# Kernel tuning notes

Hardware: AMD Instinct MI355X
Metric: run time of the kernel (lower is better)

The kernel has to match this reference:

```python
import jax, jax.numpy as jnp
import numpy as np

TEMPERATURE = 0.07
EPS = 1e-12  # F.normalize eps


def setup_inputs() -> dict:
    key = jax.random.key(0)
    kA, kB = jax.random.split(key)
    N, V, D = 4096, 2, 256
    A = jax.random.normal(kA, (N, V, D), dtype=jnp.float32)
    B = jax.random.normal(kB, (N, V, D), dtype=jnp.float32)
    return {"A": A, "B": B}


def _l2norm(x):
    n = jnp.sqrt(jnp.sum(x * x, axis=-1, keepdims=True))
    return x / jnp.maximum(n, EPS)


def _contrastive_loss(A, B, temperature):
    N, VA, D = A.shape
    VB = B.shape[1]
    # (N, V, D) -> (V*N, D), view-major, matching transpose(0,1).reshape
    Af = _l2norm(jnp.transpose(A, (1, 0, 2)).reshape(VA * N, D))
    Bf = _l2norm(jnp.transpose(B, (1, 0, 2)).reshape(VB * N, D))
    logits = Af @ Bf.T  # (VA*N, VB*N), square since VA == VB
    M = VA * N
    row = jnp.arange(M, dtype=jnp.int32)[:, None]          # (M, 1)
    cols = jnp.arange(M - 1, dtype=jnp.int32)[None, :]     # (1, M-1)
    # off-diagonal column indices for each row (skip j == i)
    cols = cols + (cols >= row).astype(jnp.int32)          # (M, M-1)
    lab = (row % N) == (cols % N)                          # positives mask
    logits_nd = jnp.take_along_axis(logits, cols, axis=1)  # diag removed
    # stable sort puts positives first (column order), negatives after ->
    # equivalent to torch.cat((pos, neg), dim=1)
    order = jnp.argsort(jnp.logical_not(lab), axis=1, stable=True)
    logits_cat = jnp.take_along_axis(logits_nd, order, axis=1) / temperature
    P = VB - 1  # positives per row after diagonal removal
    logp = jax.nn.log_softmax(logits_cat, axis=-1)
    # soft-label cross entropy: labels are 1.0 on first P columns, mean over rows
    return -jnp.mean(jnp.sum(logp[:, :P], axis=-1))


def reference(A, B):
    return _contrastive_loss(A, B, TEMPERATURE)
```

## Files before the change

kernel.cpp:

```cpp
#include <hip/hip_runtime.h>
#include <hip/hip_bf16.h>


#define N_SAMP 4096
#define DIM    256
#define M_ROWS 8192

using short8 = __attribute__((ext_vector_type(8))) short;
using f32x4  = __attribute__((ext_vector_type(4))) float;

#define GLDS(g, l) __builtin_amdgcn_global_load_lds( \
    (const __attribute__((address_space(1))) void*)(g), \
    (__attribute__((address_space(3))) void*)(l), 16, 0, 0)

__global__ __launch_bounds__(256) void norm_kernel(
    const float* __restrict__ A, const float* __restrict__ B,
    unsigned short* __restrict__ Ah, unsigned short* __restrict__ Bh,
    float* __restrict__ S)
{
  int tid = threadIdx.x;
  if (blockIdx.x < 8)
    ((float4*)S)[blockIdx.x * 256 + tid] = (float4){0.f, 0.f, 0.f, 0.f};

  int wave = tid >> 6, lane = tid & 63;
  int gw   = blockIdx.x * 4 + wave;
  const float* src; unsigned short* dst; int m;
  if (gw < M_ROWS) { src = A; dst = Ah; m = gw; }
  else             { src = B; dst = Bh; m = gw - M_ROWS; }
  int n = m & (N_SAMP - 1);
  int v = m >> 12;
  const float4* in = (const float4*)(src + (size_t)(n * 2 + v) * DIM);
  float4 x = in[lane];
  float ss = x.x*x.x + x.y*x.y + x.z*x.z + x.w*x.w;
  #pragma unroll
  for (int d = 1; d < 64; d <<= 1) ss += __shfl_xor(ss, d);
  float scale = 1.0f / fmaxf(sqrtf(ss), 1e-12f);
  float vals[4] = {x.x*scale, x.y*scale, x.z*scale, x.w*scale};
  ushort4 o;
  unsigned short* op = (unsigned short*)&o;
  #pragma unroll
  for (int k = 0; k < 4; ++k) {
    unsigned int u = __float_as_uint(vals[k]);
    u += 0x7fffu + ((u >> 16) & 1u);
    op[k] = (unsigned short)(u >> 16);
  }
  *(ushort4*)(dst + (size_t)m * DIM + lane * 4) = o;
}

__global__ __launch_bounds__(512, 2) void gemm_lse_kernel(
    const unsigned short* __restrict__ Ah, const unsigned short* __restrict__ Bh,
    float* __restrict__ S, float* __restrict__ Pos)
{
  __shared__ alignas(16) char lds[65536 + 2 * 32768];
  char* As  = lds;
  char* Bs0 = lds + 65536;
  char* Bs1 = lds + 65536 + 32768;

  int tid  = threadIdx.x;
  int lane = tid & 63;
  int w    = tid >> 6;
  int wrow = w >> 2, wcol = w & 3;
  int row0 = blockIdx.y * 128;
  int col0 = blockIdx.x * 2048;

  #pragma unroll
  for (int s = 0; s < 8; ++s) {
    int f = s * 512 + tid;
    int r = f >> 5, cd = f & 31;
    int cs = cd ^ (r & 7);
    GLDS((const char*)Ah + (size_t)(row0 + r) * 512 + cs * 16, As + f * 16);
  }
  auto stageB = [&](int t, char* Bbuf) {
    int ct = t >> 2, ks = t & 3;
    const char* base = (const char*)Bh + (size_t)(col0 + ct * 256) * 512 + ks * 128;
    #pragma unroll
    for (int s = 0; s < 4; ++s) {
      int f = s * 512 + tid;
      int r = f >> 3, cd = f & 7;
      int cs = cd ^ (r & 7);
      GLDS(base + (size_t)r * 512 + cs * 16, Bbuf + f * 16);
    }
  };
  stageB(0, Bs0);

  f32x4 acc[4][4];
  float ssum[4][4];
  #pragma unroll
  for (int i = 0; i < 4; ++i)
    #pragma unroll
    for (int r = 0; r < 4; ++r) ssum[i][r] = 0.f;

  const float KE = (float)(1.4426950408889634 / 0.07);

  for (int t = 0; t < 32; ++t) {
    char* Bcur = (t & 1) ? Bs1 : Bs0;
    char* Bnxt = (t & 1) ? Bs0 : Bs1;
    if (t < 31) {
      stageB(t + 1, Bnxt);
      asm volatile("s_waitcnt vmcnt(4)" ::: "memory");
    } else {
      asm volatile("s_waitcnt vmcnt(0)" ::: "memory");
    }
    __builtin_amdgcn_s_barrier();

    int ks = t & 3;
    if (ks == 0) {
      #pragma unroll
      for (int i = 0; i < 4; ++i)
        #pragma unroll
        for (int j = 0; j < 4; ++j)
          acc[i][j] = (f32x4){0.f, 0.f, 0.f, 0.f};
    }

    #pragma unroll
    for (int kk = 0; kk < 2; ++kk) {
      short8 a[4], b[4];
      int ca = ks * 8 + kk * 4 + (lane >> 4);
      int cb = kk * 4 + (lane >> 4);
      #pragma unroll
      for (int f = 0; f < 4; ++f) {
        int ar = wrow * 64 + f * 16 + (lane & 15);
        a[f] = *(const short8*)(As + ar * 512 + ((ca ^ (ar & 7)) * 16));
        int br = wcol * 64 + f * 16 + (lane & 15);
        b[f] = *(const short8*)(Bcur + br * 128 + ((cb ^ (br & 7)) * 16));
      }
      #pragma unroll
      for (int i = 0; i < 4; ++i)
        #pragma unroll
        for (int j = 0; j < 4; ++j)
          acc[i][j] = __builtin_amdgcn_mfma_f32_16x16x32_bf16(a[i], b[j], acc[i][j], 0, 0, 0);
    }

    if (ks == 3) {
      int ct = t >> 2;
      #pragma unroll
      for (int i = 0; i < 4; ++i) {
        #pragma unroll
        for (int j = 0; j < 4; ++j) {
          int gj = col0 + ct * 256 + wcol * 64 + j * 16 + (lane & 15);
          #pragma unroll
          for (int r = 0; r < 4; ++r) {
            int gi = row0 + wrow * 64 + i * 16 + (lane >> 4) * 4 + r;
            float l = acc[i][j][r];
            float e = exp2f(l * KE);
            if (((gi ^ gj) & (N_SAMP - 1)) == 0) {
              if (gi == gj) e = 0.f;
              else Pos[gi] = l;
            }
            ssum[i][r] += e;
          }
        }
      }
    }
    __builtin_amdgcn_s_barrier();
  }

  #pragma unroll
  for (int i = 0; i < 4; ++i) {
    #pragma unroll
    for (int r = 0; r < 4; ++r) {
      float v = ssum[i][r];
      v += __shfl_xor(v, 1);
      v += __shfl_xor(v, 2);
      v += __shfl_xor(v, 4);
      v += __shfl_xor(v, 8);
      if ((lane & 15) == 0) {
        int gi = row0 + wrow * 64 + i * 16 + (lane >> 4) * 4 + r;
        atomicAdd(&S[gi], v);
      }
    }
  }
}

__global__ __launch_bounds__(1024) void reduce_kernel(
    const float* __restrict__ S, const float* __restrict__ Pos,
    float* __restrict__ out)
{
  __shared__ float wsum[16];
  int tid = threadIdx.x;
  const float INVT = 1.0f / 0.07f;
  const float4* S4 = (const float4*)S;
  const float4* P4 = (const float4*)Pos;
  float acc = 0.f;
  #pragma unroll
  for (int q = 0; q < 2; ++q) {
    float4 s = S4[tid * 2 + q];
    float4 p = P4[tid * 2 + q];
    acc += logf(s.x) - p.x * INVT;
    acc += logf(s.y) - p.y * INVT;
    acc += logf(s.z) - p.z * INVT;
    acc += logf(s.w) - p.w * INVT;
  }
  #pragma unroll
  for (int d = 1; d < 64; d <<= 1) acc += __shfl_xor(acc, d);
  if ((tid & 63) == 0) wsum[tid >> 6] = acc;
  __syncthreads();
  if (tid == 0) {
    float t = 0.f;
    #pragma unroll
    for (int k = 0; k < 16; ++k) t += wsum[k];
    out[0] = t / (float)M_ROWS;
  }
}

extern "C" void kernel_launch(void* const* d_in, const int* in_sizes, int n_in,
                              void* d_out, int out_size, void* d_ws, size_t ws_size,
                              hipStream_t stream)
{
  const float* A = (const float*)d_in[0];
  const float* B = (const float*)d_in[1];
  char* ws = (char*)d_ws;
  unsigned short* Ah = (unsigned short*)ws;
  unsigned short* Bh = (unsigned short*)(ws + (size_t)M_ROWS * DIM * 2);
  float* S   = (float*)(ws + 2 * (size_t)M_ROWS * DIM * 2);
  float* Pos = S + M_ROWS;

  norm_kernel<<<dim3(2 * M_ROWS / 4), 256, 0, stream>>>(A, B, Ah, Bh, S);
  gemm_lse_kernel<<<dim3(4, 64), 512, 0, stream>>>(Ah, Bh, S, Pos);
  reduce_kernel<<<1, 1024, 0, stream>>>(S, Pos, (float*)d_out);
}
```

Measured before the change: 123.4 us.

## Hoist A fragments into registers and fuse final reduction via last-block atomic

Each wave now preloads all of its A-tile fragments from LDS into registers once, instead of rereading them every k-step. Positive logits are summed in registers and added atomically, so the Pos array is gone. The separate reduce kernel is replaced by a last-block-done counter pattern inside the GEMM kernel, which saves one launch. It also adds setprio and sched_barrier hints around the MFMA section. The cost is much higher register pressure, with 128 VGPRs for the A fragments, which may hurt occupancy under launch_bounds(512,2) or cause spills, plus a serial tail in the last block.

```diff
diff --git a/kernel.cpp b/kernel.cpp
--- a/kernel.cpp
+++ b/kernel.cpp
@@ -5,6 +5,7 @@
 #define N_SAMP 4096
 #define DIM    256
 #define M_ROWS 8192
+#define TEMP   0.07f
 
 using short8 = __attribute__((ext_vector_type(8))) short;
 using f32x4  = __attribute__((ext_vector_type(4))) float;
@@ -16,11 +17,12 @@
 __global__ __launch_bounds__(256) void norm_kernel(
     const float* __restrict__ A, const float* __restrict__ B,
     unsigned short* __restrict__ Ah, unsigned short* __restrict__ Bh,
-    float* __restrict__ S)
+    float* __restrict__ S, float* __restrict__ PosSum, int* __restrict__ cnt)
 {
   int tid = threadIdx.x;
   if (blockIdx.x < 8)
     ((float4*)S)[blockIdx.x * 256 + tid] = (float4){0.f, 0.f, 0.f, 0.f};
+  if (blockIdx.x == 8 && tid == 0) { PosSum[0] = 0.f; cnt[0] = 0; }
 
   int wave = tid >> 6, lane = tid & 63;
   int gw   = blockIdx.x * 4 + wave;
@@ -49,9 +51,12 @@
 
 __global__ __launch_bounds__(512, 2) void gemm_lse_kernel(
     const unsigned short* __restrict__ Ah, const unsigned short* __restrict__ Bh,
-    float* __restrict__ S, float* __restrict__ Pos)
+    float* __restrict__ S, float* __restrict__ PosSum, int* __restrict__ cnt,
+    float* __restrict__ out)
 {
   __shared__ alignas(16) char lds[65536 + 2 * 32768];
+  __shared__ float redbuf[8];
+  __shared__ int lastFlag;
   char* As  = lds;
   char* Bs0 = lds + 65536;
   char* Bs1 = lds + 65536 + 32768;
@@ -70,9 +75,21 @@
     int cs = cd ^ (r & 7);
     GLDS((const char*)Ah + (size_t)(row0 + r) * 512 + cs * 16, As + f * 16);
   }
-  auto stageB = [&](int t, char* Bbuf) {
-    int ct = t >> 2, ks = t & 3;
-    const char* base = (const char*)Bh + (size_t)(col0 + ct * 256) * 512 + ks * 128;
+  __syncthreads();
+
+  short8 a[8][4];
+  #pragma unroll
+  for (int ck = 0; ck < 8; ++ck) {
+    int ca = ck * 4 + (lane >> 4);
+    #pragma unroll
+    for (int f = 0; f < 4; ++f) {
+      int ar = wrow * 64 + f * 16 + (lane & 15);
+      a[ck][f] = *(const short8*)(As + ar * 512 + ((ca ^ (ar & 7)) * 16));
+    }
+  }
+
+  auto stageB = [&](int ctn, int ksn, char* Bbuf) {
+    const char* base = (const char*)Bh + (size_t)(col0 + ctn * 256) * 512 + ksn * 128;
     #pragma unroll
     for (int s = 0; s < 4; ++s) {
       int f = s * 512 + tid;
@@ -81,7 +98,7 @@
       GLDS(base + (size_t)r * 512 + cs * 16, Bbuf + f * 16);
     }
   };
-  stageB(0, Bs0);
+  stageB(0, 0, Bs0);
 
   f32x4 acc[4][4];
   float ssum[4][4];
@@ -89,70 +106,77 @@
   for (int i = 0; i < 4; ++i)
     #pragma unroll
     for (int r = 0; r < 4; ++r) ssum[i][r] = 0.f;
+  float psum = 0.f;
 
   const float KE = (float)(1.4426950408889634 / 0.07);
 
-  for (int t = 0; t < 32; ++t) {
-    char* Bcur = (t & 1) ? Bs1 : Bs0;
-    char* Bnxt = (t & 1) ? Bs0 : Bs1;
-    if (t < 31) {
-      stageB(t + 1, Bnxt);
-      asm volatile("s_waitcnt vmcnt(4)" ::: "memory");
-    } else {
-      asm volatile("s_waitcnt vmcnt(0)" ::: "memory");
-    }
-    __builtin_amdgcn_s_barrier();
-
-    int ks = t & 3;
-    if (ks == 0) {
+  #pragma unroll 1
+  for (int ct = 0; ct < 8; ++ct) {
+    #pragma unroll
+    for (int ks = 0; ks < 4; ++ks) {
+      char* Bcur = (ks & 1) ? Bs1 : Bs0;
+      char* Bnxt = (ks & 1) ? Bs0 : Bs1;
+      if (ks < 3) {
+        stageB(ct, ks + 1, Bnxt);
+        asm volatile("s_waitcnt vmcnt(4)" ::: "memory");
+      } else if (ct < 7) {
+        stageB(ct + 1, 0, Bnxt);
+        asm volatile("s_waitcnt vmcnt(4)" ::: "memory");
+      } else {
+        asm volatile("s_waitcnt vmcnt(0)" ::: "memory");
+      }
+      __builtin_amdgcn_s_barrier();
+      __builtin_amdgcn_sched_barrier(0);
+
+      if (ks == 0) {
+        #pragma unroll
+        for (int i = 0; i < 4; ++i)
+          #pragma unroll
+          for (int j = 0; j < 4; ++j)
+            acc[i][j] = (f32x4){0.f, 0.f, 0.f, 0.f};
+      }
+
+      __builtin_amdgcn_s_setprio(1);
       #pragma unroll
-      for (int i = 0; i < 4; ++i)
-        #pragma unroll
-        for (int j = 0; j < 4; ++j)
-          acc[i][j] = (f32x4){0.f, 0.f, 0.f, 0.f};
-    }
-
-    #pragma unroll
-    for (int kk = 0; kk < 2; ++kk) {
-      short8 a[4], b[4];
-      int ca = ks * 8 + kk * 4 + (lane >> 4);
-      int cb = kk * 4 + (lane >> 4);
-      #pragma unroll
-      for (int f = 0; f < 4; ++f) {
-        int ar = wrow * 64 + f * 16 + (lane & 15);
-        a[f] = *(const short8*)(As + ar * 512 + ((ca ^ (ar & 7)) * 16));
-        int br = wcol * 64 + f * 16 + (lane & 15);
-        b[f] = *(const short8*)(Bcur + br * 128 + ((cb ^ (br & 7)) * 16));
-      }
-      #pragma unroll
-      for (int i = 0; i < 4; ++i)
-        #pragma unroll
-        for (int j = 0; j < 4; ++j)
-          acc[i][j] = __builtin_amdgcn_mfma_f32_16x16x32_bf16(a[i], b[j], acc[i][j], 0, 0, 0);
-    }
-
-    if (ks == 3) {
-      int ct = t >> 2;
-      #pragma unroll
-      for (int i = 0; i < 4; ++i) {
-        #pragma unroll
-        for (int j = 0; j < 4; ++j) {
-          int gj = col0 + ct * 256 + wcol * 64 + j * 16 + (lane & 15);
+      for (int kk = 0; kk < 2; ++kk) {
+        short8 b[4];
+        int cb = kk * 4 + (lane >> 4);
+        #pragma unroll
+        for (int f = 0; f < 4; ++f) {
+          int br = wcol * 64 + f * 16 + (lane & 15);
+          b[f] = *(const short8*)(Bcur + br * 128 + ((cb ^ (br & 7)) * 16));
+        }
+        #pragma unroll
+        for (int i = 0; i < 4; ++i)
           #pragma unroll
-          for (int r = 0; r < 4; ++r) {
-            int gi = row0 + wrow * 64 + i * 16 + (lane >> 4) * 4 + r;
-            float l = acc[i][j][r];
-            float e = exp2f(l * KE);
-            if (((gi ^ gj) & (N_SAMP - 1)) == 0) {
-              if (gi == gj) e = 0.f;
-              else Pos[gi] = l;
+          for (int j = 0; j < 4; ++j)
+            acc[i][j] = __builtin_amdgcn_mfma_f32_16x16x32_bf16(a[ks * 2 + kk][i], b[j], acc[i][j], 0, 0, 0);
+      }
+      __builtin_amdgcn_s_setprio(0);
+
+      if (ks == 3) {
+        #pragma unroll
+        for (int i = 0; i < 4; ++i) {
+          #pragma unroll
+          for (int j = 0; j < 4; ++j) {
+            int gj = col0 + ct * 256 + wcol * 64 + j * 16 + (lane & 15);
+            #pragma unroll
+            for (int r = 0; r < 4; ++r) {
+              int gi = row0 + wrow * 64 + i * 16 + (lane >> 4) * 4 + r;
+              float l = acc[i][j][r];
+              float e = exp2f(l * KE);
+              if (((gi ^ gj) & (N_SAMP - 1)) == 0) {
+                if (gi == gj) e = 0.f;
+                else psum += l;
+              }
+              ssum[i][r] += e;
             }
-            ssum[i][r] += e;
           }
         }
       }
-    }
-    __builtin_amdgcn_s_barrier();
+      __builtin_amdgcn_s_barrier();
+      __builtin_amdgcn_sched_barrier(0);
+    }
   }
 
   #pragma unroll
@@ -170,36 +194,38 @@
       }
     }
   }
-}
-
-__global__ __launch_bounds__(1024) void reduce_kernel(
-    const float* __restrict__ S, const float* __restrict__ Pos,
-    float* __restrict__ out)
-{
-  __shared__ float wsum[16];
-  int tid = threadIdx.x;
-  const float INVT = 1.0f / 0.07f;
-  const float4* S4 = (const float4*)S;
-  const float4* P4 = (const float4*)Pos;
-  float acc = 0.f;
-  #pragma unroll
-  for (int q = 0; q < 2; ++q) {
-    float4 s = S4[tid * 2 + q];
-    float4 p = P4[tid * 2 + q];
-    acc += logf(s.x) - p.x * INVT;
-    acc += logf(s.y) - p.y * INVT;
-    acc += logf(s.z) - p.z * INVT;
-    acc += logf(s.w) - p.w * INVT;
-  }
-  #pragma unroll
-  for (int d = 1; d < 64; d <<= 1) acc += __shfl_xor(acc, d);
-  if ((tid & 63) == 0) wsum[tid >> 6] = acc;
+  float pv = psum;
+  #pragma unroll
+  for (int d = 1; d < 64; d <<= 1) pv += __shfl_xor(pv, d);
+  if (lane == 0) redbuf[w] = pv;
   __syncthreads();
   if (tid == 0) {
     float t = 0.f;
     #pragma unroll
-    for (int k = 0; k < 16; ++k) t += wsum[k];
-    out[0] = t / (float)M_ROWS;
+    for (int k = 0; k < 8; ++k) t += redbuf[k];
+    atomicAdd(PosSum, t);
+  }
+
+  __threadfence();
+  if (tid == 0) lastFlag = (atomicAdd(cnt, 1) == 255);
+  __syncthreads();
+  if (lastFlag) {
+    __threadfence();
+    float part = 0.f;
+    for (int i = tid; i < M_ROWS; i += 512)
+      part += logf(atomicAdd(&S[i], 0.0f));
+    #pragma unroll
+    for (int d = 1; d < 64; d <<= 1) part += __shfl_xor(part, d);
+    __syncthreads();
+    if (lane == 0) redbuf[w] = part;
+    __syncthreads();
+    if (tid == 0) {
+      float sl = 0.f;
+      #pragma unroll
+      for (int k = 0; k < 8; ++k) sl += redbuf[k];
+      float ps = atomicAdd(PosSum, 0.0f);
+      out[0] = sl / (float)M_ROWS - ps / ((float)M_ROWS * TEMP);
+    }
   }
 }
 
@@ -212,10 +238,10 @@
   char* ws = (char*)d_ws;
   unsigned short* Ah = (unsigned short*)ws;
   unsigned short* Bh = (unsigned short*)(ws + (size_t)M_ROWS * DIM * 2);
-  float* S   = (float*)(ws + 2 * (size_t)M_ROWS * DIM * 2);
-  float* Pos = S + M_ROWS;
-
-  norm_kernel<<<dim3(2 * M_ROWS / 4), 256, 0, stream>>>(A, B, Ah, Bh, S);
-  gemm_lse_kernel<<<dim3(4, 64), 512, 0, stream>>>(Ah, Bh, S, Pos);
-  reduce_kernel<<<1, 1024, 0, stream>>>(S, Pos, (float*)d_out);
+  float* S      = (float*)(ws + 2 * (size_t)M_ROWS * DIM * 2);
+  float* PosSum = S + M_ROWS;
+  int*   cnt    = (int*)(PosSum + 1);
+
+  norm_kernel<<<dim3(2 * M_ROWS / 4), 256, 0, stream>>>(A, B, Ah, Bh, S, PosSum, cnt);
+  gemm_lse_kernel<<<dim3(4, 64), 512, 0, stream>>>(Ah, Bh, S, PosSum, cnt, (float*)d_out);
 }
```

After: 173.6 us. 40.7% more time.
